# Optimization experiments

Measured on AMD Instinct MI355X. Metric: run time of the kernel, lower is better.

The kernel has to match this reference:

```python
import jax, jax.numpy as jnp
import numpy as np

N = 50000        # nodes
E = 1_600_000    # edges (before self-loops)
H = 2            # heads
C = 16           # out channels per head
G = 512          # graphs in batch
F_IN = 3         # const + degree + rand
NC = 2           # classes
NEG_SLOPE = 0.2  # PyG GATv2Conv default


def setup_inputs() -> dict:
    key = jax.random.key(0)
    ks = jax.random.split(key, 12)
    p = lambda k, shape: (jax.random.normal(k, shape, dtype=jnp.float32) * 0.1)
    edge_index = jax.random.randint(ks[0], (2, E), 0, N, dtype=jnp.int64)
    batch = jnp.sort(jax.random.randint(ks[1], (N,), 0, G, dtype=jnp.int64))
    rand_feat = jax.random.uniform(ks[2], (N, 1), dtype=jnp.float32)
    return {
        "edge_index": edge_index,
        "batch": batch,
        "rand_feat": rand_feat,
        # conv1: in=3 -> H*C=32
        "W1l": p(ks[3], (H * C, F_IN)), "b1l": jnp.zeros((H * C,), jnp.float32),
        "W1r": p(ks[4], (H * C, F_IN)), "b1r": jnp.zeros((H * C,), jnp.float32),
        "att1": p(ks[5], (H, C)), "bias1": jnp.zeros((H * C,), jnp.float32),
        # conv2: in=32 -> 32
        "W2l": p(ks[6], (H * C, H * C)), "b2l": jnp.zeros((H * C,), jnp.float32),
        "W2r": p(ks[7], (H * C, H * C)), "b2r": jnp.zeros((H * C,), jnp.float32),
        "att2": p(ks[8], (H, C)), "bias2": jnp.zeros((H * C,), jnp.float32),
        # fc: 32 -> 2
        "Wfc": p(ks[9], (NC, H * C)), "bfc": jnp.zeros((NC,), jnp.float32),
    }


def gatv2_conv(x, src, dst, Wl, bl, Wr, br, att, bias):
    """PyG GATv2Conv (concat=True, self-loops already appended to src/dst)."""
    n = x.shape[0]
    xl = (x @ Wl.T + bl).reshape(n, H, C)   # messages / values
    xr = (x @ Wr.T + br).reshape(n, H, C)   # target-side term
    m = xl[src] + xr[dst]                   # [E', H, C]
    e = jnp.where(m > 0, m, NEG_SLOPE * m)  # LeakyReLU
    score = jnp.einsum('ehc,hc->eh', e, att)
    # segment softmax over destination nodes (every node has a self-loop)
    smax = jax.ops.segment_max(score, dst, num_segments=n)
    ex = jnp.exp(score - smax[dst])
    denom = jax.ops.segment_sum(ex, dst, num_segments=n)
    alpha = ex / (denom[dst] + 1e-16)
    out = jax.ops.segment_sum(xl[src] * alpha[:, :, None], dst, num_segments=n)
    return out.reshape(n, H * C) + bias


def reference(edge_index, batch, rand_feat, W1l, b1l, W1r, b1r, att1, bias1,
              W2l, b2l, W2r, b2r, att2, bias2, Wfc, bfc):
    src, dst = edge_index[0], edge_index[1]
    # degree feature: index_add of ones over both rows (original edges only)
    ones_e = jnp.ones((E,), jnp.float32)
    deg = (jax.ops.segment_sum(ones_e, src, num_segments=N)
           + jax.ops.segment_sum(ones_e, dst, num_segments=N))
    x = jnp.concatenate([jnp.ones((N, 1), jnp.float32), deg[:, None], rand_feat], axis=1)
    # PyG GATv2Conv adds self-loops by default
    loops = jnp.arange(N, dtype=src.dtype)
    src_sl = jnp.concatenate([src, loops])
    dst_sl = jnp.concatenate([dst, loops])
    x = jax.nn.elu(gatv2_conv(x, src_sl, dst_sl, W1l, b1l, W1r, b1r, att1, bias1))
    x = jax.nn.elu(gatv2_conv(x, src_sl, dst_sl, W2l, b2l, W2r, b2r, att2, bias2))
    # global mean pool over graphs
    sums = jax.ops.segment_sum(x, batch, num_segments=G)
    counts = jax.ops.segment_sum(jnp.ones((N,), jnp.float32), batch, num_segments=G)
    pooled = sums / jnp.clip(counts, 1.0)[:, None]
    logits = pooled @ Wfc.T + bfc
    return jax.nn.log_softmax(logits, axis=1)
```

## Files before the change

### kernel.cpp

```cpp
#include <hip/hip_runtime.h>
#include <hip/hip_fp16.h>
#include <math.h>

#define HC 32
#define CH 16
#define NSLOPE 0.2f
#define NB2MAX 512
#define TILE 8192
#define CBMAX 5120
#define NSL 64
#define HGRP 8
#define HLDS 12544

__device__ __forceinline__ unsigned gen_pair(const int* __restrict__ ei, int E, int i){
    if (i < E) return (unsigned(ei[E+i]) << 16) | unsigned(ei[i]);
    unsigned n = i - E; return (n << 16) | n;
}

__device__ __forceinline__ __half2 pkmax2(__half2 a, __half2 b){
    union { __half2 h; unsigned u; } ua, ub, ud;
    ua.h = a; ub.h = b;
    asm("v_pk_max_f16 %0, %1, %2" : "=v"(ud.u) : "v"(ua.u), "v"(ub.u));
    return ud.h;
}

__device__ __forceinline__ __half2 sfx2(__half2 x, int off){
    union { __half2 h; int i; } u; u.h = x;
    u.i = __shfl_xor(u.i, off);
    return u.h;
}

__global__ __launch_bounds__(512) void k_front(const int* __restrict__ ei, int E, int EP,
                        int halfN, unsigned* __restrict__ hb, unsigned* __restrict__ gPair,
                        int* __restrict__ gcur, unsigned* __restrict__ part){
    __shared__ unsigned smem[14848];
    int t = threadIdx.x;
    int blk = blockIdx.x;

    if (blk < NSL*2){
        unsigned* h  = smem;
        unsigned* hp = smem + HLDS;
        int nWloc = halfN >> 1;
        for (int i = t; i < nWloc; i += 512) h[i] = 0;
        int p = blk & 1;
        if (p == 0){ hp[t] = 0; hp[t] = 0; }
        __syncthreads();
        int slice = blk >> 1;
        int base  = p * halfN;
        int chunk = (((E + NSL - 1) / NSL) + 3) & ~3;
        int lo = slice*chunk, hi = lo + chunk; if (hi > E) hi = E;
        bool v4 = ((E & 3) == 0);
        if (v4 && lo < hi){
            int m4 = lo + ((hi - lo) & ~3);
            for (int i = lo + 4*t; i + 3 < hi; i += 4*512){
                int4 s4 = *(const int4*)(ei + i);
                int a0 = s4.x - base, a1 = s4.y - base, a2 = s4.z - base, a3 = s4.w - base;
                if ((unsigned)a0 < (unsigned)halfN) atomicAdd(&h[a0 >> 1], 1u << (16*(a0 & 1)));
                if ((unsigned)a1 < (unsigned)halfN) atomicAdd(&h[a1 >> 1], 1u << (16*(a1 & 1)));
                if ((unsigned)a2 < (unsigned)halfN) atomicAdd(&h[a2 >> 1], 1u << (16*(a2 & 1)));
                if ((unsigned)a3 < (unsigned)halfN) atomicAdd(&h[a3 >> 1], 1u << (16*(a3 & 1)));
                if (p == 0){
                    int4 d4 = *(const int4*)(ei + E + i);
                    atomicAdd(&hp[unsigned(d4.x) >> 7], 1u);
                    atomicAdd(&hp[unsigned(d4.y) >> 7], 1u);
                    atomicAdd(&hp[unsigned(d4.z) >> 7], 1u);
                    atomicAdd(&hp[unsigned(d4.w) >> 7], 1u);
                }
            }
            for (int i = m4 + t; i < hi; i += 512){
                int s = ei[i] - base;
                if ((unsigned)s < (unsigned)halfN) atomicAdd(&h[s >> 1], 1u << (16*(s & 1)));
                if (p == 0) atomicAdd(&hp[unsigned(ei[E+i]) >> 7], 1u);
            }
        } else {
            for (int i = lo + t; i < hi; i += 512){
                int s = ei[i] - base;
                if ((unsigned)s < (unsigned)halfN) atomicAdd(&h[s >> 1], 1u << (16*(s & 1)));
                if (p == 0) atomicAdd(&hp[unsigned(ei[E+i]) >> 7], 1u);
            }
        }
        __syncthreads();
        unsigned* out = hb + (size_t)blk * nWloc;
        for (int w = t; w < nWloc; w += 512) out[w] = h[w];
        if (p == 0 && hp[t]) atomicAdd(&gPair[t], hp[t]);
    } else {
        int* bcnt   = (int*)smem;
        int* bstart = bcnt + 512;
        int* c2     = bstart + 512;
        int* gpos   = c2 + 512;
        int* sc     = gpos + 512;
        unsigned* sorted = (unsigned*)(sc + 512);
        unsigned short* bktof = (unsigned short*)(sorted + TILE);
        int tile = blk - NSL*2;
        int base = tile * TILE;
        int cnt = EP - base; if (cnt > TILE) cnt = TILE;
        bool full = (cnt == TILE);
        bcnt[t] = 0; c2[t] = 0;
        __syncthreads();
        unsigned ec[TILE/512];
        if (full){
            #pragma unroll
            for (int q = 0; q < TILE/512; ++q)
                ec[q] = gen_pair(ei, E, base + t + q*512);
            #pragma unroll
            for (int q = 0; q < TILE/512; ++q)
                atomicAdd(&bcnt[ec[q] >> 23], 1);
        } else {
            for (int j = t; j < cnt; j += 512){
                unsigned e = gen_pair(ei, E, base + j);
                atomicAdd(&bcnt[e >> 23], 1);
            }
        }
        __syncthreads();
        int v = bcnt[t];
        sc[t] = v;
        __syncthreads();
        for (int d = 1; d < 512; d <<= 1){
            int x = (t >= d) ? sc[t-d] : 0;
            __syncthreads();
            sc[t] += x;
            __syncthreads();
        }
        int excl = sc[t] - v;
        bstart[t] = excl;
        if (v > 0){
            gpos[t] = atomicAdd(&gcur[t], v);
            for (int j = 0; j < v; ++j) bktof[excl + j] = (unsigned short)t;
        }
        __syncthreads();
        if (full){
            #pragma unroll
            for (int q = 0; q < TILE/512; ++q){
                unsigned e = ec[q];
                int b = e >> 23;
                int off = atomicAdd(&c2[b], 1);
                sorted[bstart[b] + off] = e;
            }
        } else {
            for (int j = t; j < cnt; j += 512){
                unsigned e = gen_pair(ei, E, base + j);
                int b = e >> 23;
                int off = atomicAdd(&c2[b], 1);
                sorted[bstart[b] + off] = e;
            }
        }
        __syncthreads();
        for (int k = t; k < cnt; k += 512){
            int b = bktof[k];
            int rel = gpos[b] + (k - bstart[b]);
            if (rel < CBMAX) part[(size_t)b*CBMAX + rel] = sorted[k];
        }
    }
}

__global__ void k_back(const unsigned* __restrict__ hb, unsigned* __restrict__ degS,
                       int nWloc, const int* __restrict__ batch, int* __restrict__ gb,
                       int N, int G, int nHred,
                       unsigned* __restrict__ gPair, int* __restrict__ partBase,
                       int* __restrict__ rsN, int EP, int nb,
                       const float* __restrict__ W1l, const float* __restrict__ b1l,
                       const float* __restrict__ W1r, const float* __restrict__ b1r,
                       const float* __restrict__ att1, const float* __restrict__ bias1,
                       float4* __restrict__ tabA, float4* __restrict__ tabB){
    __shared__ int sc[256];
    int t = threadIdx.x;
    int blk = blockIdx.x;
    if (blk < nHred){
        int idx = blk*256 + t;
        if (idx <= G){
            int lo = 0, hi = N;
            while (lo < hi){ int mid = (lo+hi)>>1; if (batch[mid] < idx) lo = mid+1; else hi = mid; }
            gb[idx] = lo;
        }
        int total = 2*nWloc;
        int grp = idx / total;
        if (grp < HGRP){
            int rem = idx - grp*total;
            int p = (rem < nWloc) ? 0 : 1;
            int w = rem - p*nWloc;
            unsigned s = 0;
            int sl0 = grp*(NSL/HGRP), sl1 = sl0 + NSL/HGRP;
            for (int sl = sl0; sl < sl1; ++sl)
                s += hb[(size_t)(sl*2 + p)*nWloc + w];
            if (s) atomicAdd(&degS[rem], s);
        }
    } else {
        int vp0 = 0, vp1 = 0;
        int b0 = 2*t, b1 = 2*t + 1;
        if (b0 < nb){
            int selfc = N - b0*128;
            selfc = (selfc < 0) ? 0 : (selfc > 128 ? 128 : selfc);
            vp0 = (int)gPair[b0] + selfc;
            gPair[b0] = (unsigned)vp0;
        }
        if (b1 < nb){
            int selfc = N - b1*128;
            selfc = (selfc < 0) ? 0 : (selfc > 128 ? 128 : selfc);
            vp1 = (int)gPair[b1] + selfc;
            gPair[b1] = (unsigned)vp1;
        }
        int s = vp0 + vp1;
        sc[t] = s;
        __syncthreads();
        for (int d = 1; d < 256; d <<= 1){
            int x = (t >= d) ? sc[t-d] : 0;
            __syncthreads();
            sc[t] += x;
            __syncthreads();
        }
        int excl = sc[t] - s;
        if (b0 < nb) partBase[b0] = excl;
        if (b1 < nb) partBase[b1] = excl + vp0;
        if (t == 0) rsN[0] = EP;
        if (t < HC){
            tabA[t] = make_float4(W1l[t*3] + b1l[t], W1l[t*3+1], W1l[t*3+2], att1[t]);
            tabB[t] = make_float4(W1r[t*3] + b1r[t], W1r[t*3+1], W1r[t*3+2], bias1[t]);
        }
    }
}

__global__ void k_fine(const unsigned* __restrict__ part, const int* __restrict__ partBase,
                       const unsigned* __restrict__ gPair,
                       const unsigned* __restrict__ degS, const float* __restrict__ rnd,
                       int* __restrict__ rs, float2* __restrict__ dr,
                       int* __restrict__ col, int N){
    __shared__ int pcnt[128], c2[128], lrs[129], sc[128];
    __shared__ int colbuf[CBMAX];
    int b = blockIdx.x, t = threadIdx.x;
    int np = (int)gPair[b]; if (np > CBMAX) np = CBMAX;
    int beg = b*CBMAX, end = beg + np;
    if (t < 128){ pcnt[t] = 0; c2[t] = 0; }
    __syncthreads();
    for (int k = beg + t; k < end; k += 256)
        atomicAdd(&pcnt[(part[k] >> 16) & 127], 1);
    __syncthreads();
    int v = (t < 128) ? pcnt[t] : 0;
    if (t < 128) sc[t] = v;
    __syncthreads();
    for (int d = 1; d < 128; d <<= 1){
        int x = (t >= d && t < 128) ? sc[t-d] : 0;
        __syncthreads();
        if (t < 128) sc[t] += x;
        __syncthreads();
    }
    if (t < 128){
        lrs[t] = sc[t] - v;
        if (t == 127) lrs[128] = sc[127];
    }
    __syncthreads();
    int n = (b << 7) + t;
    int pb = partBase[b];
    if (t < 128 && n < N){
        rs[n] = pb + lrs[t];
        unsigned s16 = (degS[n >> 1] >> (16*(n & 1))) & 0xFFFFu;
        dr[n] = make_float2((float)(pcnt[t] - 1 + (int)s16), rnd[n]);
    }
    for (int k = beg + t; k < end; k += 256){
        unsigned e = part[k];
        int j = (e >> 16) & 127;
        int pos = lrs[j] + atomicAdd(&c2[j], 1);
        if (pos < CBMAX) colbuf[pos] = (int)(e & 0xFFFFu);
    }
    __syncthreads();
    int npair = lrs[128];
    for (int k = t; k < npair; k += 256) col[pb + k] = colbuf[k];
}

__global__ void k_gat1(const int* __restrict__ rs, const int* __restrict__ col,
                       const float2* __restrict__ dr,
                       const float4* __restrict__ tabA, const float4* __restrict__ tabB,
                       const float* __restrict__ W2l, const float* __restrict__ b2l,
                       const float* __restrict__ W2r, const float* __restrict__ b2r,
                       __half* __restrict__ A16, __half* __restrict__ B16, int N){
    __shared__ float4 tA[HC], tB[HC];
    __shared__ float4 wq[HC][16];
    __shared__ float blS[HC], brS[HC];
    int t = threadIdx.x;
    if (t < HC){ tA[t] = tabA[t]; tB[t] = tabB[t]; blS[t] = b2l[t]; brS[t] = b2r[t]; }
    for (int w = t; w < HC*16; w += 256){
        int j = w >> 4, k = w & 15;
        wq[j][k] = make_float4(W2l[(2*k)*HC + j], W2l[(2*k+1)*HC + j],
                               W2r[(2*k)*HC + j], W2r[(2*k+1)*HC + j]);
    }
    __syncthreads();

    int d = blockIdx.x*(blockDim.x >> 4) + (t >> 4);
    if (d >= N) return;
    int lane = t & 15;
    int h = lane >> 3, r = lane & 7;

    float2 drd = dr[d];
    float base[CH];
    #pragma unroll
    for (int c = 0; c < CH; ++c){
        float4 a4 = tA[h*CH + c];
        float4 b4 = tB[h*CH + c];
        float xr = b4.x + b4.y*drd.x + b4.z*drd.y;
        base[c] = a4.x + xr;
    }

    float l = 0.f, S1 = 0.f, S2 = 0.f;
    int beg = rs[d], end = rs[d+1];
    int p = beg + r;
    for (; p + 8 < end; p += 16){
        int s0 = __builtin_nontemporal_load(col + p);
        int s1 = __builtin_nontemporal_load(col + p + 8);
        float2 da = dr[s0];
        float2 db = dr[s1];
        float sc0 = 0.f, sc1 = 0.f;
        #pragma unroll
        for (int c = 0; c < CH; ++c){
            float4 a4 = tA[h*CH + c];
            float m0 = base[c] + a4.y*da.x + a4.z*da.y;
            float m1 = base[c] + a4.y*db.x + a4.z*db.y;
            m0 = (m0 > 0.f) ? m0 : NSLOPE*m0;
            m1 = (m1 > 0.f) ? m1 : NSLOPE*m1;
            sc0 += m0 * a4.w;
            sc1 += m1 * a4.w;
        }
        float ex0 = __expf(sc0), ex1 = __expf(sc1);
        l  += ex0 + ex1;
        S1 += ex0*da.x + ex1*db.x;
        S2 += ex0*da.y + ex1*db.y;
    }
    if (p < end){
        float2 ds = dr[__builtin_nontemporal_load(col + p)];
        float sc = 0.f;
        #pragma unroll
        for (int c = 0; c < CH; ++c){
            float4 a4 = tA[h*CH + c];
            float mm = base[c] + a4.y*ds.x + a4.z*ds.y;
            mm = (mm > 0.f) ? mm : NSLOPE*mm;
            sc += mm * a4.w;
        }
        float ex = __expf(sc);
        l  += ex;
        S1 += ex*ds.x;
        S2 += ex*ds.y;
    }

    #pragma unroll
    for (int off = 4; off >= 1; off >>= 1){
        l  += __shfl_xor(l,  off);
        S1 += __shfl_xor(S1, off);
        S2 += __shfl_xor(S2, off);
    }

    float invl = 1.f/(l + 1e-16f);
    int c0 = r*2;
    float4 a40 = tA[h*CH + c0],     b40 = tB[h*CH + c0];
    float4 a41 = tA[h*CH + c0 + 1], b41 = tB[h*CH + c0 + 1];
    float v0 = a40.x + (a40.y*S1 + a40.z*S2)*invl + b40.w;
    float v1 = a41.x + (a41.y*S1 + a41.z*S2)*invl + b41.w;
    float x0 = (v0 > 0.f) ? v0 : expm1f(v0);
    float x1 = (v1 > 0.f) ? v1 : expm1f(v1);

    int k0 = 2*lane;
    float a0 = blS[k0], a1 = blS[k0+1];
    float g0 = brS[k0], g1 = brS[k0+1];
    #pragma unroll
    for (int tt = 0; tt < 16; ++tt){
        float xa = __shfl(x0, tt, 16);
        float xb = __shfl(x1, tt, 16);
        int j = 2*tt;
        float4 q0 = wq[j][lane];
        float4 q1 = wq[j+1][lane];
        a0 += xa*q0.x + xb*q1.x;
        a1 += xa*q0.y + xb*q1.y;
        g0 += xa*q0.z + xb*q1.z;
        g1 += xa*q0.w + xb*q1.w;
    }
    *(__half2*)(A16 + (size_t)d*HC + k0) = __floats2half2_rn(a0, a1);
    *(__half2*)(B16 + (size_t)d*HC + k0) = __floats2half2_rn(g0, g1);
}

__global__ void k_gat(const int* __restrict__ rs, const int* __restrict__ col,
                      const __half* __restrict__ A16, const __half* __restrict__ B16,
                      const float* __restrict__ att, const float* __restrict__ bias,
                      const int* __restrict__ batch, float* __restrict__ pooled, int N){
    __shared__ float pool[8][HC];
    __shared__ int sb[8];
    int sg = threadIdx.x >> 5;
    int d = blockIdx.x*(blockDim.x >> 5) + sg;
    int lane = threadIdx.x & 31;
    bool valid = (d < N);
    int dcl = valid ? d : 0;
    int h = lane >> 4, r = lane & 15;

    union U { uint4 u[2]; __half2 h2[8]; };
    U xr;
    {
        const uint4* bp = (const uint4*)(B16 + (size_t)dcl*HC + h*CH);
        xr.u[0] = bp[0]; xr.u[1] = bp[1];
    }
    __half2 at2[8];
    const float* atf = att + h*CH;
    #pragma unroll
    for (int i = 0; i < 8; ++i) at2[i] = __floats2half2_rn(atf[2*i], atf[2*i+1]);
    const __half2 ns2 = __float2half2_rn(NSLOPE);

    float l = 0.f;
    __half2 acc2[8];
    #pragma unroll
    for (int i = 0; i < 8; ++i) acc2[i] = __float2half2_rn(0.f);

    int beg = rs[dcl], end = valid ? rs[dcl+1] : beg;
    int p = beg + r;
    for (; p + 16 < end; p += 32){
        int s0 = __builtin_nontemporal_load(col + p);
        int s1 = __builtin_nontemporal_load(col + p + 16);
        const uint4* rp0 = (const uint4*)(A16 + (size_t)s0*HC + h*CH);
        const uint4* rp1 = (const uint4*)(A16 + (size_t)s1*HC + h*CH);
        U a, b;
        a.u[0] = rp0[0]; a.u[1] = rp0[1];
        b.u[0] = rp1[0]; b.u[1] = rp1[1];
        __half2 sc2 = __float2half2_rn(0.f);
        #pragma unroll
        for (int i = 0; i < 8; ++i){
            __half2 m  = __hadd2(a.h2[i], xr.h2[i]);
            __half2 lk = pkmax2(m, __hmul2(m, ns2));
            sc2 = __hfma2(lk, at2[i], sc2);
        }
        float ex = __expf(__low2float(sc2) + __high2float(sc2));
        l += ex;
        __half2 exh = __float2half2_rn(ex);
        #pragma unroll
        for (int i = 0; i < 8; ++i) acc2[i] = __hfma2(a.h2[i], exh, acc2[i]);

        sc2 = __float2half2_rn(0.f);
        #pragma unroll
        for (int i = 0; i < 8; ++i){
            __half2 m  = __hadd2(b.h2[i], xr.h2[i]);
            __half2 lk = pkmax2(m, __hmul2(m, ns2));
            sc2 = __hfma2(lk, at2[i], sc2);
        }
        ex = __expf(__low2float(sc2) + __high2float(sc2));
        l += ex;
        exh = __float2half2_rn(ex);
        #pragma unroll
        for (int i = 0; i < 8; ++i) acc2[i] = __hfma2(b.h2[i], exh, acc2[i]);
    }
    if (p < end){
        int s = __builtin_nontemporal_load(col + p);
        const uint4* rp = (const uint4*)(A16 + (size_t)s*HC + h*CH);
        U a;
        a.u[0] = rp[0]; a.u[1] = rp[1];
        __half2 sc2 = __float2half2_rn(0.f);
        #pragma unroll
        for (int i = 0; i < 8; ++i){
            __half2 m  = __hadd2(a.h2[i], xr.h2[i]);
            __half2 lk = pkmax2(m, __hmul2(m, ns2));
            sc2 = __hfma2(lk, at2[i], sc2);
        }
        float ex = __expf(__low2float(sc2) + __high2float(sc2));
        l += ex;
        __half2 exh = __float2half2_rn(ex);
        #pragma unroll
        for (int i = 0; i < 8; ++i) acc2[i] = __hfma2(a.h2[i], exh, acc2[i]);
    }

    __half2 v4[4];
    {
        bool hi = (r & 8) != 0;
        #pragma unroll
        for (int i = 0; i < 4; ++i){
            __half2 send = hi ? acc2[i] : acc2[i+4];
            __half2 recv = sfx2(send, 8);
            v4[i] = __hadd2(hi ? acc2[i+4] : acc2[i], recv);
        }
    }
    __half2 v2[2];
    {
        bool hi = (r & 4) != 0;
        __half2 s0 = hi ? v4[0] : v4[2];
        __half2 s1 = hi ? v4[1] : v4[3];
        __half2 r0 = sfx2(s0, 4);
        __half2 r1 = sfx2(s1, 4);
        v2[0] = __hadd2(hi ? v4[2] : v4[0], r0);
        v2[1] = __hadd2(hi ? v4[3] : v4[1], r1);
    }
    __half2 v1;
    {
        bool hi = (r & 2) != 0;
        __half2 send = hi ? v2[0] : v2[1];
        __half2 recv = sfx2(send, 2);
        v1 = __hadd2(hi ? v2[1] : v2[0], recv);
    }
    float mine;
    {
        bool hi = (r & 1) != 0;
        float lo = __low2float(v1), hf = __high2float(v1);
        float send = hi ? lo : hf;
        float recv = __shfl_xor(send, 1);
        mine = (hi ? hf : lo) + recv;
    }
    #pragma unroll
    for (int off = 8; off >= 1; off >>= 1) l += __shfl_xor(l, off);

    float invl = 1.f/(l + 1e-16f);
    float val = mine*invl + bias[h*CH + r];
    val = (val > 0.f) ? val : expm1f(val);

    if (lane == 0) sb[sg] = valid ? batch[d] : (-1 - sg);
    pool[sg][h*CH + r] = val;
    __syncthreads();
    int myb = sb[sg];
    int first = sg;
    #pragma unroll
    for (int j = 7; j >= 0; --j) if (sb[j] == myb) first = j;
    if (valid && first == sg){
        float s = 0.f;
        #pragma unroll
        for (int j = 0; j < 8; ++j) if (sb[j] == myb) s += pool[j][h*CH + r];
        atomicAdd(&pooled[(size_t)myb*HC + h*CH + r], s);
    }
}

__global__ void k_fc(const float* __restrict__ pooled, const int* __restrict__ gb,
                     const float* __restrict__ Wfc, const float* __restrict__ bfc,
                     float* __restrict__ out, int G){
    int t = threadIdx.x;
    int g = blockIdx.x*2 + (t >> 5);
    int c = t & 31;
    if (g >= G) return;
    float cnt = (float)(gb[g+1] - gb[g]);
    if (cnt < 1.f) cnt = 1.f;
    float pv = pooled[g*HC + c] / cnt;
    float p0 = pv * Wfc[c];
    float p1 = pv * Wfc[HC + c];
    #pragma unroll
    for (int off = 16; off >= 1; off >>= 1){
        p0 += __shfl_xor(p0, off, 32);
        p1 += __shfl_xor(p1, off, 32);
    }
    if (c == 0){
        float l0 = p0 + bfc[0], l1 = p1 + bfc[1];
        float m = (l0 > l1) ? l0 : l1;
        float lse = m + logf(__expf(l0 - m) + __expf(l1 - m));
        out[g*2 + 0] = l0 - lse;
        out[g*2 + 1] = l1 - lse;
    }
}

extern "C" void kernel_launch(void* const* d_in, const int* in_sizes, int n_in,
                              void* d_out, int out_size, void* d_ws, size_t ws_size,
                              hipStream_t stream) {
    const int*   ei    = (const int*)  d_in[0];
    const int*   batch = (const int*)  d_in[1];
    const float* rnd   = (const float*)d_in[2];
    const float* W1l   = (const float*)d_in[3];
    const float* b1l   = (const float*)d_in[4];
    const float* W1r   = (const float*)d_in[5];
    const float* b1r   = (const float*)d_in[6];
    const float* att1  = (const float*)d_in[7];
    const float* bias1 = (const float*)d_in[8];
    const float* W2l   = (const float*)d_in[9];
    const float* b2l   = (const float*)d_in[10];
    const float* W2r   = (const float*)d_in[11];
    const float* b2r   = (const float*)d_in[12];
    const float* att2  = (const float*)d_in[13];
    const float* bias2 = (const float*)d_in[14];
    const float* Wfc   = (const float*)d_in[15];
    const float* bfc   = (const float*)d_in[16];

    const int E  = in_sizes[0] / 2;
    const int N  = in_sizes[1];
    const int G  = out_size / 2;
    const int EP = E + N;
    const int NB2 = (N + 127) >> 7;
    const int halfN = (((N + 1) >> 1) + 1) & ~1;
    const int nWloc = halfN >> 1;

    float* ws        = (float*)d_ws;
    __half* A16      = (__half*)ws;
    __half* B16      = A16 + (size_t)N*HC;
    unsigned* hb     = (unsigned*)ws;
    size_t off1      = (size_t)NSL*2*nWloc;
    if (off1 < (size_t)N*HC) off1 = (size_t)N*HC;
    unsigned* part   = (unsigned*)ws + off1;
    size_t off2      = off1 + (size_t)NB2*CBMAX;
    off2 = (off2 + 1) & ~(size_t)1;
    float2* dr       = (float2*)(ws + off2);
    int*   rs        = (int*)(dr + N);
    int*   col       = rs + N + 1;
    unsigned* degS   = (unsigned*)(col + EP);
    unsigned* gPair  = degS + 2*nWloc;
    float* pooled    = (float*)(gPair + NB2MAX);
    int*   gcur      = (int*)(pooled + (size_t)G*HC);
    int*   partBase  = gcur + NB2MAX;
    int*   gb        = partBase + NB2MAX;
    float4* tabA     = (float4*)((((size_t)(gb + G + 1)) + 15) & ~(size_t)15);
    float4* tabB     = tabA + HC;

    const int T = 256;
    const int gD16 = (N + (T>>4) - 1)/(T>>4);
    const int gD32 = (N + (T>>5) - 1)/(T>>5);
    const int nTiles = (EP + TILE - 1)/TILE;
    const int nHred  = (2*nWloc*HGRP + T-1)/T;

    (void)hipMemsetAsync(degS, 0,
        (size_t)(2*nWloc + NB2MAX + (size_t)G*HC + NB2MAX)*sizeof(unsigned), stream);

    k_front<<<NSL*2 + nTiles, 512, 0, stream>>>(ei, E, EP, halfN, hb, gPair, gcur, part);
    k_back <<<nHred + 1, T, 0, stream>>>(hb, degS, nWloc, batch, gb, N, G, nHred,
                                   gPair, partBase, rs + N, EP, NB2,
                                   W1l, b1l, W1r, b1r, att1, bias1, tabA, tabB);
    k_fine <<<NB2, T, 0, stream>>>(part, partBase, gPair, degS, rnd, rs, dr, col, N);

    k_gat1<<<gD16, T, 0, stream>>>(rs, col, dr, tabA, tabB,
                                   W2l, b2l, W2r, b2r, A16, B16, N);

    k_gat <<<gD32, T, 0, stream>>>(rs, col, A16, B16, att2, bias2, batch, pooled, N);

    k_fc  <<<(G + 1)/2, 64, 0, stream>>>(pooled, gb, Wfc, bfc, (float*)d_out, G);
}
```

Baseline: 201.3 us.

## Eliminate k_back kernel by folding its work into k_front and k_fine

```diff
diff --git a/kernel.cpp b/kernel.cpp
--- a/kernel.cpp
+++ b/kernel.cpp
@@ -9,7 +9,6 @@
 #define TILE 8192
 #define CBMAX 5120
 #define NSL 64
-#define HGRP 8
 #define HLDS 12544
 
 __device__ __forceinline__ unsigned gen_pair(const int* __restrict__ ei, int E, int i){
@@ -32,7 +31,9 @@
 
 __global__ __launch_bounds__(512) void k_front(const int* __restrict__ ei, int E, int EP,
                         int halfN, unsigned* __restrict__ hb, unsigned* __restrict__ gPair,
-                        int* __restrict__ gcur, unsigned* __restrict__ part){
+                        int* __restrict__ gcur, unsigned* __restrict__ part,
+                        const int* __restrict__ batch, int* __restrict__ gb,
+                        int N, int G, int nTiles){
     __shared__ unsigned smem[14848];
     int t = threadIdx.x;
     int blk = blockIdx.x;
@@ -43,7 +44,7 @@
         int nWloc = halfN >> 1;
         for (int i = t; i < nWloc; i += 512) h[i] = 0;
         int p = blk & 1;
-        if (p == 0){ hp[t] = 0; hp[t] = 0; }
+        if (p == 0) hp[t] = 0;
         __syncthreads();
         int slice = blk >> 1;
         int base  = p * halfN;
@@ -83,7 +84,7 @@
         unsigned* out = hb + (size_t)blk * nWloc;
         for (int w = t; w < nWloc; w += 512) out[w] = h[w];
         if (p == 0 && hp[t]) atomicAdd(&gPair[t], hp[t]);
-    } else {
+    } else if (blk < NSL*2 + nTiles){
         int* bcnt   = (int*)smem;
         int* bstart = bcnt + 512;
         int* c2     = bstart + 512;
@@ -150,86 +151,59 @@
             int rel = gpos[b] + (k - bstart[b]);
             if (rel < CBMAX) part[(size_t)b*CBMAX + rel] = sorted[k];
         }
-    }
-}
-
-__global__ void k_back(const unsigned* __restrict__ hb, unsigned* __restrict__ degS,
-                       int nWloc, const int* __restrict__ batch, int* __restrict__ gb,
-                       int N, int G, int nHred,
-                       unsigned* __restrict__ gPair, int* __restrict__ partBase,
-                       int* __restrict__ rsN, int EP, int nb,
-                       const float* __restrict__ W1l, const float* __restrict__ b1l,
-                       const float* __restrict__ W1r, const float* __restrict__ b1r,
-                       const float* __restrict__ att1, const float* __restrict__ bias1,
-                       float4* __restrict__ tabA, float4* __restrict__ tabB){
-    __shared__ int sc[256];
-    int t = threadIdx.x;
-    int blk = blockIdx.x;
-    if (blk < nHred){
-        int idx = blk*256 + t;
+    } else {
+        int idx = (blk - NSL*2 - nTiles)*512 + t;
         if (idx <= G){
             int lo = 0, hi = N;
             while (lo < hi){ int mid = (lo+hi)>>1; if (batch[mid] < idx) lo = mid+1; else hi = mid; }
             gb[idx] = lo;
         }
-        int total = 2*nWloc;
-        int grp = idx / total;
-        if (grp < HGRP){
-            int rem = idx - grp*total;
-            int p = (rem < nWloc) ? 0 : 1;
-            int w = rem - p*nWloc;
-            unsigned s = 0;
-            int sl0 = grp*(NSL/HGRP), sl1 = sl0 + NSL/HGRP;
-            for (int sl = sl0; sl < sl1; ++sl)
-                s += hb[(size_t)(sl*2 + p)*nWloc + w];
-            if (s) atomicAdd(&degS[rem], s);
-        }
-    } else {
-        int vp0 = 0, vp1 = 0;
-        int b0 = 2*t, b1 = 2*t + 1;
-        if (b0 < nb){
-            int selfc = N - b0*128;
-            selfc = (selfc < 0) ? 0 : (selfc > 128 ? 128 : selfc);
-            vp0 = (int)gPair[b0] + selfc;
-            gPair[b0] = (unsigned)vp0;
-        }
-        if (b1 < nb){
-            int selfc = N - b1*128;
-            selfc = (selfc < 0) ? 0 : (selfc > 128 ? 128 : selfc);
-            vp1 = (int)gPair[b1] + selfc;
-            gPair[b1] = (unsigned)vp1;
-        }
-        int s = vp0 + vp1;
-        sc[t] = s;
-        __syncthreads();
-        for (int d = 1; d < 256; d <<= 1){
-            int x = (t >= d) ? sc[t-d] : 0;
-            __syncthreads();
-            sc[t] += x;
-            __syncthreads();
-        }
-        int excl = sc[t] - s;
-        if (b0 < nb) partBase[b0] = excl;
-        if (b1 < nb) partBase[b1] = excl + vp0;
-        if (t == 0) rsN[0] = EP;
-        if (t < HC){
-            tabA[t] = make_float4(W1l[t*3] + b1l[t], W1l[t*3+1], W1l[t*3+2], att1[t]);
-            tabB[t] = make_float4(W1r[t*3] + b1r[t], W1r[t*3+1], W1r[t*3+2], bias1[t]);
-        }
-    }
-}
-
-__global__ void k_fine(const unsigned* __restrict__ part, const int* __restrict__ partBase,
-                       const unsigned* __restrict__ gPair,
-                       const unsigned* __restrict__ degS, const float* __restrict__ rnd,
+    }
+}
+
+__global__ void k_fine(const unsigned* __restrict__ part, const unsigned* __restrict__ hb,
+                       const unsigned* __restrict__ gPair, int halfN,
+                       const float* __restrict__ rnd,
                        int* __restrict__ rs, float2* __restrict__ dr,
-                       int* __restrict__ col, int N){
-    __shared__ int pcnt[128], c2[128], lrs[129], sc[128];
+                       int* __restrict__ col, int N, int EP){
+    __shared__ int pcnt[128], c2[128], lrs[129], sc[128], sdeg[128], redbuf[256];
     __shared__ int colbuf[CBMAX];
     int b = blockIdx.x, t = threadIdx.x;
-    int np = (int)gPair[b]; if (np > CBMAX) np = CBMAX;
+    int nWloc = halfN >> 1;
+
+    int acc = 0;
+    for (int j = t; j < b; j += 256) acc += (int)gPair[j];
+    redbuf[t] = acc;
+    __syncthreads();
+    for (int s = 128; s > 0; s >>= 1){
+        if (t < s) redbuf[t] += redbuf[t+s];
+        __syncthreads();
+    }
+    int selfpre = b*128; if (selfpre > N) selfpre = N;
+    int pb = redbuf[0] + selfpre;
+    int selfc = N - b*128; selfc = (selfc < 0) ? 0 : (selfc > 128 ? 128 : selfc);
+    int np = (int)gPair[b] + selfc; if (np > CBMAX) np = CBMAX;
+    __syncthreads();
+
+    {
+        int node = t & 127, half = t >> 7;
+        int n = (b << 7) + node;
+        unsigned sum = 0;
+        if (n < N){
+            int pn = (n >= halfN) ? 1 : 0;
+            int idx = n - pn*halfN;
+            int w = idx >> 1, sh = 16*(idx & 1);
+            int sl0 = half*(NSL/2), sl1 = sl0 + NSL/2;
+            for (int sl = sl0; sl < sl1; ++sl)
+                sum += (hb[(size_t)(sl*2 + pn)*nWloc + w] >> sh) & 0xFFFFu;
+        }
+        redbuf[t] = (int)sum;
+    }
+    if (t < 128){ pcnt[t] = 0; c2[t] = 0; }
+    __syncthreads();
+    if (t < 128) sdeg[t] = redbuf[t] + redbuf[t+128];
+
     int beg = b*CBMAX, end = beg + np;
-    if (t < 128){ pcnt[t] = 0; c2[t] = 0; }
     __syncthreads();
     for (int k = beg + t; k < end; k += 256)
         atomicAdd(&pcnt[(part[k] >> 16) & 127], 1);
@@ -249,12 +223,11 @@
     }
     __syncthreads();
     int n = (b << 7) + t;
-    int pb = partBase[b];
     if (t < 128 && n < N){
         rs[n] = pb + lrs[t];
-        unsigned s16 = (degS[n >> 1] >> (16*(n & 1))) & 0xFFFFu;
-        dr[n] = make_float2((float)(pcnt[t] - 1 + (int)s16), rnd[n]);
-    }
+        dr[n] = make_float2((float)(pcnt[t] - 1 + sdeg[t]), rnd[n]);
+    }
+    if (b == 0 && t == 0) rs[N] = EP;
     for (int k = beg + t; k < end; k += 256){
         unsigned e = part[k];
         int j = (e >> 16) & 127;
@@ -268,7 +241,9 @@
 
 __global__ void k_gat1(const int* __restrict__ rs, const int* __restrict__ col,
                        const float2* __restrict__ dr,
-                       const float4* __restrict__ tabA, const float4* __restrict__ tabB,
+                       const float* __restrict__ W1l, const float* __restrict__ b1l,
+                       const float* __restrict__ W1r, const float* __restrict__ b1r,
+                       const float* __restrict__ att1, const float* __restrict__ bias1,
                        const float* __restrict__ W2l, const float* __restrict__ b2l,
                        const float* __restrict__ W2r, const float* __restrict__ b2r,
                        __half* __restrict__ A16, __half* __restrict__ B16, int N){
@@ -276,7 +251,11 @@
     __shared__ float4 wq[HC][16];
     __shared__ float blS[HC], brS[HC];
     int t = threadIdx.x;
-    if (t < HC){ tA[t] = tabA[t]; tB[t] = tabB[t]; blS[t] = b2l[t]; brS[t] = b2r[t]; }
+    if (t < HC){
+        tA[t] = make_float4(W1l[t*3] + b1l[t], W1l[t*3+1], W1l[t*3+2], att1[t]);
+        tB[t] = make_float4(W1r[t*3] + b1r[t], W1r[t*3+1], W1r[t*3+2], bias1[t]);
+        blS[t] = b2l[t]; brS[t] = b2r[t];
+    }
     for (int w = t; w < HC*16; w += 256){
         int j = w >> 4, k = w & 15;
         wq[j][k] = make_float4(W2l[(2*k)*HC + j], W2l[(2*k+1)*HC + j],
@@ -583,31 +562,26 @@
     float2* dr       = (float2*)(ws + off2);
     int*   rs        = (int*)(dr + N);
     int*   col       = rs + N + 1;
-    unsigned* degS   = (unsigned*)(col + EP);
-    unsigned* gPair  = degS + 2*nWloc;
+    unsigned* gPair  = (unsigned*)(col + EP);
     float* pooled    = (float*)(gPair + NB2MAX);
     int*   gcur      = (int*)(pooled + (size_t)G*HC);
-    int*   partBase  = gcur + NB2MAX;
-    int*   gb        = partBase + NB2MAX;
-    float4* tabA     = (float4*)((((size_t)(gb + G + 1)) + 15) & ~(size_t)15);
-    float4* tabB     = tabA + HC;
+    int*   gb        = gcur + NB2MAX;
 
     const int T = 256;
     const int gD16 = (N + (T>>4) - 1)/(T>>4);
     const int gD32 = (N + (T>>5) - 1)/(T>>5);
     const int nTiles = (EP + TILE - 1)/TILE;
-    const int nHred  = (2*nWloc*HGRP + T-1)/T;
-
-    (void)hipMemsetAsync(degS, 0,
-        (size_t)(2*nWloc + NB2MAX + (size_t)G*HC + NB2MAX)*sizeof(unsigned), stream);
-
-    k_front<<<NSL*2 + nTiles, 512, 0, stream>>>(ei, E, EP, halfN, hb, gPair, gcur, part);
-    k_back <<<nHred + 1, T, 0, stream>>>(hb, degS, nWloc, batch, gb, N, G, nHred,
-                                   gPair, partBase, rs + N, EP, NB2,
-                                   W1l, b1l, W1r, b1r, att1, bias1, tabA, tabB);
-    k_fine <<<NB2, T, 0, stream>>>(part, partBase, gPair, degS, rnd, rs, dr, col, N);
-
-    k_gat1<<<gD16, T, 0, stream>>>(rs, col, dr, tabA, tabB,
+    const int nGb    = (G + 1 + 511)/512;
+
+    (void)hipMemsetAsync(gPair, 0,
+        (size_t)(NB2MAX + (size_t)G*HC + NB2MAX)*sizeof(unsigned), stream);
+
+    k_front<<<NSL*2 + nTiles + nGb, 512, 0, stream>>>(ei, E, EP, halfN, hb, gPair,
+                                   gcur, part, batch, gb, N, G, nTiles);
+    k_fine <<<NB2, T, 0, stream>>>(part, hb, gPair, halfN, rnd, rs, dr, col, N, EP);
+
+    k_gat1<<<gD16, T, 0, stream>>>(rs, col, dr,
+                                   W1l, b1l, W1r, b1r, att1, bias1,
                                    W2l, b2l, W2r, b2r, A16, B16, N);
 
     k_gat <<<gD32, T, 0, stream>>>(rs, col, A16, B16, att2, bias2, batch, pooled, N);
```

New measurement: 201.0 us. No clear change (-0.2%).
